# Optimization experiments

Hardware: AMD Instinct MI355X
Metric: run time of the kernel (lower is better)

## Reference

```python
import jax, jax.numpy as jnp
import numpy as np

N = 524288
MAXV = 8  # rect-rect intersection has at most 8 vertices
EPS = 1e-8


def setup_inputs() -> dict:
    key = jax.random.key(0)
    k1, k2, k3 = jax.random.split(key, 3)
    return {
        "box": jax.random.normal(k1, (N, 11), jnp.float32),
        "box_target": jax.random.normal(k2, (N, 11), jnp.float32),
        "weight": jax.random.uniform(k3, (N, 11), jnp.float32),
        "avg_factor": N // 2,
    }


def decode_box(box):
    # [x,y,z,logW,logL,logH,sin,cos,v...] -> [x,y,z,W,L,H,yaw,v...]
    yaw = jnp.arctan2(box[..., 6], box[..., 7])
    return jnp.concatenate(
        [box[..., :3], jnp.exp(box[..., 3:6]), yaw[..., None], box[..., 8:]], axis=-1)


def get_rect_vertices(bev):
    # bev: (5,) = [cx, cy, w, l, yaw] -> (4, 2) corners, CCW, rotated about center
    cx, cy, w, l, yaw = bev[0], bev[1], bev[2], bev[3], bev[4]
    dx, dy = w / 2, l / 2
    lx = jnp.stack([-dx, dx, dx, -dx])
    ly = jnp.stack([-dy, -dy, dy, dy])
    s, c = jnp.sin(yaw), jnp.cos(yaw)
    return jnp.stack([lx * c - ly * s + cx, lx * s + ly * c + cy], axis=-1)


def clip_halfplane(poly, count, a, b):
    # Sutherland-Hodgman clip of poly (MAXV,2) with `count` valid verts
    # against left side of directed edge a->b. Fixed-size buffer + mask.
    d = b - a  # (2,)
    idx = jnp.arange(MAXV)
    cnt = jnp.maximum(count, 1)
    prev = poly[(idx - 1) % cnt]
    cur = poly

    def is_left(p):
        return d[0] * (p[..., 1] - a[1]) - d[1] * (p[..., 0] - a[0]) >= 0

    cur_in, prev_in = is_left(cur), is_left(prev)
    num = (a[0] - prev[:, 0]) * d[1] - (a[1] - prev[:, 1]) * d[0]
    den = (cur[:, 0] - prev[:, 0]) * d[1] - (cur[:, 1] - prev[:, 1]) * d[0] + EPS
    ip = prev + (num / den)[:, None] * (cur - prev)  # edge/halfplane intersection
    valid = idx < count
    emit_ip = valid & (prev_in ^ cur_in)   # crossing edge -> emit intersection
    emit_cur = valid & cur_in              # inside vertex -> emit it
    # interleave per-input-edge outputs in original order (ip, then cur)
    pts = jnp.stack([ip, cur], axis=1).reshape(2 * MAXV, 2)
    emit = jnp.stack([emit_ip, emit_cur], axis=1).reshape(2 * MAXV)
    pos = jnp.where(emit, jnp.cumsum(emit) - 1, MAXV)  # compact valid pts to front
    out = jnp.zeros((MAXV, 2), poly.dtype).at[pos].set(
        jnp.where(emit[:, None], pts, 0.0), mode="drop")
    return out, jnp.minimum(emit.sum(), MAXV).astype(jnp.int32)


def poly_area(poly, count):
    # shoelace over the `count` valid vertices
    idx = jnp.arange(MAXV)
    nxt = poly[(idx + 1) % jnp.maximum(count, 1)]
    cross = jnp.where(idx < count, poly[:, 0] * nxt[:, 1] - poly[:, 1] * nxt[:, 0], 0.0)
    return jnp.abs(cross.sum() / 2.0)


def giou_one(bev1, bev2):
    v1 = get_rect_vertices(bev1)  # (4,2)
    v2 = get_rect_vertices(bev2)
    poly = jnp.zeros((MAXV, 2), bev1.dtype).at[:4].set(v1)
    count = jnp.int32(4)
    for i in range(4):  # clip subject rect by 4 half-planes of clip rect
        poly, count = clip_halfplane(poly, count, v2[i], v2[(i + 1) % 4])
        count = jnp.where(count < 3, 0, count)  # degenerate -> empty (original break)
    inter = poly_area(poly, count)
    area1 = bev1[2] * bev1[3]
    area2 = bev2[2] * bev2[3]
    union = area1 + area2 - inter
    allp = jnp.concatenate([v1, v2], axis=0)
    enclosing = (allp[:, 0].max() - allp[:, 0].min()) * (allp[:, 1].max() - allp[:, 1].min())
    iou = inter / (union + EPS)
    return iou - (enclosing - union) / (enclosing + EPS)


def _bev(dec):
    return jnp.stack([dec[:, 0], dec[:, 1], dec[:, 3], dec[:, 4], dec[:, 6]], axis=-1)


def reference(box, box_target, weight, avg_factor):
    af = max(float(avg_factor), 1.0)
    # L1 box loss (reg_weights are all 1.0 per init defaults)
    loss_box = (jnp.abs(box - box_target) * weight).sum() / af
    # rotated BEV GIoU loss
    bev_p = _bev(decode_box(box))
    bev_t = _bev(decode_box(box_target))
    giou = jax.vmap(giou_one)(bev_p, bev_t)
    loss_giou = (1.0 - giou).sum() / af
    return loss_box, loss_giou
```

## Files before the change

### kernel.cpp

```cpp
#include <hip/hip_runtime.h>

#define BLOCK 256
#define EPSF 1e-8f

__device__ __forceinline__ void lb_clip(float px, float py, float dx, float dy,
                                        float hx, float hy,
                                        float& tmin, float& tmax) {
    float sdx = (fabsf(dx) > 1e-30f) ? dx : copysignf(1e-30f, dx);
    float sdy = (fabsf(dy) > 1e-30f) ? dy : copysignf(1e-30f, dy);
    float rdx = __frcp_rn(sdx);
    float rdy = __frcp_rn(sdy);
    float t1x = (-hx - px) * rdx, t2x = (hx - px) * rdx;
    float t1y = (-hy - py) * rdy, t2y = (hy - py) * rdy;
    tmin = fmaxf(fmaxf(fminf(t1x, t2x), fminf(t1y, t2y)), 0.f);
    tmax = fminf(fminf(fmaxf(t1x, t2x), fmaxf(t1y, t2y)), 1.f);
}

__global__ __launch_bounds__(BLOCK) void box_loss_main(
    const float* __restrict__ box, const float* __restrict__ tgt,
    const float* __restrict__ wgt, int n, float* __restrict__ partials)
{
    __shared__ __align__(16) float stage[5632];
    __shared__ float red[8];

    const int tid  = threadIdx.x;
    const int slab = blockIdx.x * BLOCK;
    const int slabN = min(BLOCK, n - slab);
    const size_t g0 = (size_t)slab * 11;

    float l1sum = 0.f;
    if (slabN == BLOCK) {
        const float4* b4 = (const float4*)(box + g0);
        const float4* t4 = (const float4*)(tgt + g0);
        const float4* w4 = (const float4*)(wgt + g0);
        float4* sb4 = (float4*)stage;
        float4* st4 = (float4*)(stage + 2816);
#pragma unroll
        for (int k = 0; k < 3; ++k) {
            int idx = tid + k * BLOCK;
            if (idx < 704) {
                float4 vb = b4[idx], vt = t4[idx], vw = w4[idx];
                l1sum += fabsf(vb.x - vt.x) * vw.x + fabsf(vb.y - vt.y) * vw.y
                       + fabsf(vb.z - vt.z) * vw.z + fabsf(vb.w - vt.w) * vw.w;
                sb4[idx] = vb;
                st4[idx] = vt;
            }
        }
    } else {
        const int F = slabN * 11;
        for (int j = tid; j < F; j += BLOCK) {
            float bb = box[g0 + j], tt = tgt[g0 + j], ww = wgt[g0 + j];
            l1sum += fabsf(bb - tt) * ww;
            stage[j] = bb; stage[2816 + j] = tt;
        }
    }
    __syncthreads();

    float giou_term = 0.f;
    if (tid < slabN) {
        const int b = tid * 11, t = 2816 + b;
        float cx1 = stage[b + 0], cy1 = stage[b + 1];
        float lw1 = stage[b + 3], ll1 = stage[b + 4];
        float sy1 = stage[b + 6], cw1 = stage[b + 7];
        float cx2 = stage[t + 0], cy2 = stage[t + 1];
        float lw2 = stage[t + 3], ll2 = stage[t + 4];
        float sy2 = stage[t + 6], cw2 = stage[t + 7];

        float w1 = __expf(lw1), l1v = __expf(ll1);
        float w2 = __expf(lw2), l2v = __expf(ll2);
        float r1 = rsqrtf(fmaxf(sy1 * sy1 + cw1 * cw1, 1e-30f));
        float s1 = sy1 * r1, c1 = cw1 * r1;
        float r2 = rsqrtf(fmaxf(sy2 * sy2 + cw2 * cw2, 1e-30f));
        float s2 = sy2 * r2, c2 = cw2 * r2;

        float hx1 = 0.5f * w1, hy1 = 0.5f * l1v;
        float hx2 = 0.5f * w2, hy2 = 0.5f * l2v;

        float e1x = fabsf(hx1 * c1) + fabsf(hy1 * s1);
        float e1y = fabsf(hx1 * s1) + fabsf(hy1 * c1);
        float e2x = fabsf(hx2 * c2) + fabsf(hy2 * s2);
        float e2y = fabsf(hx2 * s2) + fabsf(hy2 * c2);
        float enc = (fmaxf(cx1 + e1x, cx2 + e2x) - fminf(cx1 - e1x, cx2 - e2x))
                  * (fmaxf(cy1 + e1y, cy2 + e2y) - fminf(cy1 - e1y, cy2 - e2y));

        float dxw = cx1 - cx2, dyw = cy1 - cy2;
        float txl =  c2 * dxw + s2 * dyw;
        float tyl = -s2 * dxw + c2 * dyw;
        float cr_ = c1 * c2 + s1 * s2;
        float sr_ = s1 * c2 - c1 * s2;

        const float UX[4] = { -1.f, 1.f, 1.f, -1.f };
        const float UY[4] = { -1.f, -1.f, 1.f, 1.f };
        float qx[4], qy[4];
#pragma unroll
        for (int k = 0; k < 4; ++k) {
            float ux = UX[k] * hx1, uy = UY[k] * hy1;
            qx[k] = txl + ux * cr_ - uy * sr_;
            qy[k] = tyl + ux * sr_ + uy * cr_;
        }

        float inter2 = 0.f;

#pragma unroll
        for (int k = 0; k < 4; ++k) {
            int kn = (k + 1) & 3;
            float px = qx[k], py = qy[k];
            float dx = qx[kn] - px, dy = qy[kn] - py;
            float t0, t1;
            lb_clip(px, py, dx, dy, hx2, hy2, t0, t1);
            float ax = fmaf(t0, dx, px), ay = fmaf(t0, dy, py);
            float bx = fmaf(t1, dx, px), by = fmaf(t1, dy, py);
            float c = ax * by - ay * bx;
            inter2 += (t1 > t0) ? c : 0.f;
        }

        {
            float Rx[4] = { -hx2, hx2, hx2, -hx2 };
            float Ry[4] = { -hy2, -hy2, hy2, hy2 };
            float ux[4], uy[4];
#pragma unroll
            for (int k = 0; k < 4; ++k) {
                float zx = Rx[k] - txl, zy = Ry[k] - tyl;
                ux[k] =  cr_ * zx + sr_ * zy;
                uy[k] = -sr_ * zx + cr_ * zy;
            }
#pragma unroll
            for (int k = 0; k < 4; ++k) {
                int kn = (k + 1) & 3;
                float du = ux[kn] - ux[k], dv = uy[kn] - uy[k];
                float t0, t1;
                lb_clip(ux[k], uy[k], du, dv, hx1, hy1, t0, t1);
                float dzx = Rx[kn] - Rx[k], dzy = Ry[kn] - Ry[k];
                float ax = fmaf(t0, dzx, Rx[k]), ay = fmaf(t0, dzy, Ry[k]);
                float bx = fmaf(t1, dzx, Rx[k]), by = fmaf(t1, dzy, Ry[k]);
                float c = ax * by - ay * bx;
                inter2 += (t1 > t0) ? c : 0.f;
            }
        }

        float inter = 0.5f * fabsf(inter2);

        float areaU = w1 * l1v + w2 * l2v - inter;
        float iou = inter / (areaU + EPSF);
        float giou = iou - (enc - areaU) / (enc + EPSF);
        giou_term = 1.f - giou;
    }

    float sb = l1sum, sg = giou_term;
#pragma unroll
    for (int off = 32; off > 0; off >>= 1) {
        sb += __shfl_down(sb, off);
        sg += __shfl_down(sg, off);
    }
    const int wave = tid >> 6, lane = tid & 63;
    if (lane == 0) { red[wave] = sb; red[4 + wave] = sg; }
    __syncthreads();
    if (tid == 0) {
        float a = red[0] + red[1] + red[2] + red[3];
        float g = red[4] + red[5] + red[6] + red[7];
        partials[2 * (size_t)blockIdx.x]     = a;
        partials[2 * (size_t)blockIdx.x + 1] = g;
    }
}

__global__ __launch_bounds__(256) void box_loss_final(
    const float* __restrict__ partials, int nblk,
    const int* __restrict__ avg_factor, float* __restrict__ out)
{
    __shared__ float red[8];
    float a = 0.f, g = 0.f;
    for (int i = threadIdx.x; i < nblk; i += 256) {
        a += partials[2 * (size_t)i];
        g += partials[2 * (size_t)i + 1];
    }
#pragma unroll
    for (int off = 32; off > 0; off >>= 1) {
        a += __shfl_down(a, off);
        g += __shfl_down(g, off);
    }
    const int wave = threadIdx.x >> 6, lane = threadIdx.x & 63;
    if (lane == 0) { red[wave] = a; red[4 + wave] = g; }
    __syncthreads();
    if (threadIdx.x == 0) {
        float af = (float)(*avg_factor);
        if (af < 1.f) af = 1.f;
        out[0] = (red[0] + red[1] + red[2] + red[3]) / af;
        out[1] = (red[4] + red[5] + red[6] + red[7]) / af;
    }
}

extern "C" void kernel_launch(void* const* d_in, const int* in_sizes, int n_in,
                              void* d_out, int out_size, void* d_ws, size_t ws_size,
                              hipStream_t stream) {
    const float* box = (const float*)d_in[0];
    const float* tgt = (const float*)d_in[1];
    const float* wgt = (const float*)d_in[2];
    const int*   af  = (const int*)d_in[3];
    float* out = (float*)d_out;
    float* partials = (float*)d_ws;

    int n = in_sizes[0] / 11;
    int nblk = (n + BLOCK - 1) / BLOCK;
    if (nblk < 1) nblk = 1;

    hipLaunchKernelGGL(box_loss_main, dim3(nblk), dim3(BLOCK), 0, stream,
                       box, tgt, wgt, n, partials);
    hipLaunchKernelGGL(box_loss_final, dim3(1), dim3(256), 0, stream,
                       partials, nblk, af, out);
}
```

Before: 23.81 us.

## Fuse final reduction via atomics and use grid-stride loop with direct per-thread loads

Replaces the two-kernel partial-sum plus final-reduce scheme with a single grid-stride kernel that accumulates per block and atomically adds scaled sums into the output after a memset. Each thread now loads its 11-float rows directly from global memory instead of staging them through LDS with coalesced float4 loads. The grid is capped at 512 blocks. The aim is to remove the second launch and the LDS staging, but the strided 44-byte per-thread loads may coalesce worse, and float atomics make the summation order nondeterministic.

```diff
diff --git a/kernel.cpp b/kernel.cpp
--- a/kernel.cpp
+++ b/kernel.cpp
@@ -1,6 +1,7 @@
 #include <hip/hip_runtime.h>
 
 #define BLOCK 256
+#define NBLK  512
 #define EPSF 1e-8f
 
 __device__ __forceinline__ void lb_clip(float px, float py, float dx, float dy,
@@ -16,62 +17,36 @@
     tmax = fminf(fminf(fmaxf(t1x, t2x), fmaxf(t1y, t2y)), 1.f);
 }
 
-__global__ __launch_bounds__(BLOCK) void box_loss_main(
+__global__ __launch_bounds__(BLOCK) void box_loss_fused(
     const float* __restrict__ box, const float* __restrict__ tgt,
-    const float* __restrict__ wgt, int n, float* __restrict__ partials)
+    const float* __restrict__ wgt, int n,
+    const int* __restrict__ avg_factor, float* __restrict__ out)
 {
-    __shared__ __align__(16) float stage[5632];
     __shared__ float red[8];
 
-    const int tid  = threadIdx.x;
-    const int slab = blockIdx.x * BLOCK;
-    const int slabN = min(BLOCK, n - slab);
-    const size_t g0 = (size_t)slab * 11;
+    const int tid = threadIdx.x;
+    const int stride = gridDim.x * BLOCK;
+    float sumL1 = 0.f, sumG = 0.f;
 
-    float l1sum = 0.f;
-    if (slabN == BLOCK) {
-        const float4* b4 = (const float4*)(box + g0);
-        const float4* t4 = (const float4*)(tgt + g0);
-        const float4* w4 = (const float4*)(wgt + g0);
-        float4* sb4 = (float4*)stage;
-        float4* st4 = (float4*)(stage + 2816);
+    for (int i = blockIdx.x * BLOCK + tid; i < n; i += stride) {
+        const float* bp = box + (size_t)i * 11;
+        const float* tp = tgt + (size_t)i * 11;
+        const float* wp = wgt + (size_t)i * 11;
+        float b[11], t[11], w[11];
 #pragma unroll
-        for (int k = 0; k < 3; ++k) {
-            int idx = tid + k * BLOCK;
-            if (idx < 704) {
-                float4 vb = b4[idx], vt = t4[idx], vw = w4[idx];
-                l1sum += fabsf(vb.x - vt.x) * vw.x + fabsf(vb.y - vt.y) * vw.y
-                       + fabsf(vb.z - vt.z) * vw.z + fabsf(vb.w - vt.w) * vw.w;
-                sb4[idx] = vb;
-                st4[idx] = vt;
-            }
-        }
-    } else {
-        const int F = slabN * 11;
-        for (int j = tid; j < F; j += BLOCK) {
-            float bb = box[g0 + j], tt = tgt[g0 + j], ww = wgt[g0 + j];
-            l1sum += fabsf(bb - tt) * ww;
-            stage[j] = bb; stage[2816 + j] = tt;
-        }
-    }
-    __syncthreads();
+        for (int j = 0; j < 11; ++j) { b[j] = bp[j]; t[j] = tp[j]; w[j] = wp[j]; }
 
-    float giou_term = 0.f;
-    if (tid < slabN) {
-        const int b = tid * 11, t = 2816 + b;
-        float cx1 = stage[b + 0], cy1 = stage[b + 1];
-        float lw1 = stage[b + 3], ll1 = stage[b + 4];
-        float sy1 = stage[b + 6], cw1 = stage[b + 7];
-        float cx2 = stage[t + 0], cy2 = stage[t + 1];
-        float lw2 = stage[t + 3], ll2 = stage[t + 4];
-        float sy2 = stage[t + 6], cw2 = stage[t + 7];
+        float lb = 0.f;
+#pragma unroll
+        for (int j = 0; j < 11; ++j) lb += fabsf(b[j] - t[j]) * w[j];
+        sumL1 += lb;
 
-        float w1 = __expf(lw1), l1v = __expf(ll1);
-        float w2 = __expf(lw2), l2v = __expf(ll2);
-        float r1 = rsqrtf(fmaxf(sy1 * sy1 + cw1 * cw1, 1e-30f));
-        float s1 = sy1 * r1, c1 = cw1 * r1;
-        float r2 = rsqrtf(fmaxf(sy2 * sy2 + cw2 * cw2, 1e-30f));
-        float s2 = sy2 * r2, c2 = cw2 * r2;
+        float w1 = __expf(b[3]), l1v = __expf(b[4]);
+        float w2 = __expf(t[3]), l2v = __expf(t[4]);
+        float r1 = rsqrtf(fmaxf(b[6] * b[6] + b[7] * b[7], 1e-30f));
+        float s1 = b[6] * r1, c1 = b[7] * r1;
+        float r2 = rsqrtf(fmaxf(t[6] * t[6] + t[7] * t[7], 1e-30f));
+        float s2 = t[6] * r2, c2 = t[7] * r2;
 
         float hx1 = 0.5f * w1, hy1 = 0.5f * l1v;
         float hx2 = 0.5f * w2, hy2 = 0.5f * l2v;
@@ -80,6 +55,7 @@
         float e1y = fabsf(hx1 * s1) + fabsf(hy1 * c1);
         float e2x = fabsf(hx2 * c2) + fabsf(hy2 * s2);
         float e2y = fabsf(hx2 * s2) + fabsf(hy2 * c2);
+        float cx1 = b[0], cy1 = b[1], cx2 = t[0], cy2 = t[1];
         float enc = (fmaxf(cx1 + e1x, cx2 + e2x) - fminf(cx1 - e1x, cx2 - e2x))
                   * (fmaxf(cy1 + e1y, cy2 + e2y) - fminf(cy1 - e1y, cy2 - e2y));
 
@@ -100,7 +76,6 @@
         }
 
         float inter2 = 0.f;
-
 #pragma unroll
         for (int k = 0; k < 4; ++k) {
             int kn = (k + 1) & 3;
@@ -113,7 +88,6 @@
             float c = ax * by - ay * bx;
             inter2 += (t1 > t0) ? c : 0.f;
         }
-
         {
             float Rx[4] = { -hx2, hx2, hx2, -hx2 };
             float Ry[4] = { -hy2, -hy2, hy2, hy2 };
@@ -137,55 +111,30 @@
                 inter2 += (t1 > t0) ? c : 0.f;
             }
         }
-
         float inter = 0.5f * fabsf(inter2);
 
         float areaU = w1 * l1v + w2 * l2v - inter;
         float iou = inter / (areaU + EPSF);
         float giou = iou - (enc - areaU) / (enc + EPSF);
-        giou_term = 1.f - giou;
+        sumG += 1.f - giou;
     }
 
-    float sb = l1sum, sg = giou_term;
 #pragma unroll
     for (int off = 32; off > 0; off >>= 1) {
-        sb += __shfl_down(sb, off);
-        sg += __shfl_down(sg, off);
+        sumL1 += __shfl_down(sumL1, off);
+        sumG  += __shfl_down(sumG, off);
     }
     const int wave = tid >> 6, lane = tid & 63;
-    if (lane == 0) { red[wave] = sb; red[4 + wave] = sg; }
+    if (lane == 0) { red[wave] = sumL1; red[4 + wave] = sumG; }
     __syncthreads();
     if (tid == 0) {
-        float a = red[0] + red[1] + red[2] + red[3];
-        float g = red[4] + red[5] + red[6] + red[7];
-        partials[2 * (size_t)blockIdx.x]     = a;
-        partials[2 * (size_t)blockIdx.x + 1] = g;
-    }
-}
-
-__global__ __launch_bounds__(256) void box_loss_final(
-    const float* __restrict__ partials, int nblk,
-    const int* __restrict__ avg_factor, float* __restrict__ out)
-{
-    __shared__ float red[8];
-    float a = 0.f, g = 0.f;
-    for (int i = threadIdx.x; i < nblk; i += 256) {
-        a += partials[2 * (size_t)i];
-        g += partials[2 * (size_t)i + 1];
-    }
-#pragma unroll
-    for (int off = 32; off > 0; off >>= 1) {
-        a += __shfl_down(a, off);
-        g += __shfl_down(g, off);
-    }
-    const int wave = threadIdx.x >> 6, lane = threadIdx.x & 63;
-    if (lane == 0) { red[wave] = a; red[4 + wave] = g; }
-    __syncthreads();
-    if (threadIdx.x == 0) {
         float af = (float)(*avg_factor);
         if (af < 1.f) af = 1.f;
-        out[0] = (red[0] + red[1] + red[2] + red[3]) / af;
-        out[1] = (red[4] + red[5] + red[6] + red[7]) / af;
+        float inv = 1.f / af;
+        float a = (red[0] + red[1] + red[2] + red[3]) * inv;
+        float g = (red[4] + red[5] + red[6] + red[7]) * inv;
+        atomicAdd(&out[0], a);
+        atomicAdd(&out[1], g);
     }
 }
 
@@ -197,14 +146,14 @@
     const float* wgt = (const float*)d_in[2];
     const int*   af  = (const int*)d_in[3];
     float* out = (float*)d_out;
-    float* partials = (float*)d_ws;
 
     int n = in_sizes[0] / 11;
-    int nblk = (n + BLOCK - 1) / BLOCK;
+    int nblk = NBLK;
+    int maxblk = (n + BLOCK - 1) / BLOCK;
+    if (nblk > maxblk) nblk = maxblk;
     if (nblk < 1) nblk = 1;
 
-    hipLaunchKernelGGL(box_loss_main, dim3(nblk), dim3(BLOCK), 0, stream,
-                       box, tgt, wgt, n, partials);
-    hipLaunchKernelGGL(box_loss_final, dim3(1), dim3(256), 0, stream,
-                       partials, nblk, af, out);
+    hipMemsetAsync(out, 0, 2 * sizeof(float), stream);
+    hipLaunchKernelGGL(box_loss_fused, dim3(nblk), dim3(BLOCK), 0, stream,
+                       box, tgt, wgt, n, af, out);
 }
```

Result: slower. 33.30 us (+39.9%).
